# Optimization experiments

Hardware: AMD Instinct MI355X
Metric: run time of the kernel (lower is better)

Reference implementation:

```python
import jax, jax.numpy as jnp
import numpy as np


def setup_inputs() -> dict:
    key = jax.random.key(0)
    x = jax.random.normal(key, (4096, 16384), dtype=jnp.float32)
    return {"x": x, "k": 64}


def reference(x, k):
    # TopK activation: keep the k largest-|value| entries per row, zero the rest.
    if k <= 0:
        return jnp.zeros_like(x)
    kk = min(k, x.shape[-1])
    _, idx = jax.lax.top_k(jnp.abs(x), kk)          # idx: [rows, kk]
    rows = jnp.arange(x.shape[0])[:, None]          # [rows, 1]
    mask = jnp.zeros_like(x).at[rows, idx].set(1.0)  # scatter ones at top-k positions
    return x * mask
```

## Files before the change

kernel.cpp:

```cpp
#include <hip/hip_runtime.h>

#define ROW_LEN 16384
#define THREADS 256
#define ITERS (ROW_LEN / (THREADS * 4))
#define NBINS 2048
#define CAP 1024
#define MBCAP 128
#define TPRE 2.5f

typedef float f4v __attribute__((ext_vector_type(4)));

__device__ __forceinline__ unsigned long long make_key(unsigned abits, unsigned idx) {
    return ((unsigned long long)abits << 32) | (unsigned)(~idx);
}

__device__ __forceinline__ void find_boundary(const unsigned* hist, unsigned kk,
                                              int* s_b, unsigned* s_g, unsigned* wtot) {
    const int t = threadIdx.x;
    const int lane = t & 63;
    const int w = t >> 6;
    unsigned s_own = 0;
    #pragma unroll
    for (int i = 0; i < 8; ++i) s_own += hist[t * 8 + i];
    unsigned acc = s_own;
    #pragma unroll
    for (int off = 1; off < 64; off <<= 1) {
        unsigned v = __shfl_down(acc, off);
        if (lane + off < 64) acc += v;
    }
    if (lane == 0) wtot[w] = acc;
    __syncthreads();
    unsigned addw = 0;
    #pragma unroll
    for (int w2 = 0; w2 < THREADS / 64; ++w2) if (w2 > w) addw += wtot[w2];
    unsigned above = acc - s_own + addw;
    #pragma unroll
    for (int i = 7; i >= 0; --i) {
        unsigned h = hist[t * 8 + i];
        if (above < kk && above + h >= kk) { *s_b = t * 8 + i; *s_g = above; }
        above += h;
    }
    __syncthreads();
}

__global__ __launch_bounds__(THREADS)
void topk_act_kernel(const float* __restrict__ x, const int* __restrict__ kptr,
                     float* __restrict__ out)
{
    const int t = threadIdx.x;
    const long long row = blockIdx.x;
    const f4v* __restrict__ xv = (const f4v*)(x + row * ROW_LEN);
    f4v* __restrict__ ov = (f4v*)(out + row * ROW_LEN);

    const int k = *kptr;
    if (k <= 0) {
        f4v z = (f4v)(0.0f);
        #pragma unroll
        for (int j = 0; j < ITERS; ++j)
            __builtin_nontemporal_store(z, &ov[j * THREADS + t]);
        return;
    }
    const unsigned kk = (unsigned)(k < ROW_LEN ? k : ROW_LEN);

    __shared__ unsigned hist[NBINS];
    __shared__ unsigned long long lst[CAP];
    __shared__ unsigned long long lst2[MBCAP];
    __shared__ unsigned wtot[THREADS / 64];
    __shared__ unsigned s_cnt, s_cnt2;
    __shared__ int s_b;
    __shared__ unsigned s_g;
    __shared__ unsigned long long s_ccut;

    if (t == 0) { s_cnt = 0u; s_cnt2 = 0u; }
    __syncthreads();

    const unsigned abs_pre = __float_as_uint(TPRE);
    for (int it = 0; it < ITERS; ++it) {
        f4v v = xv[it * THREADS + t];
        #pragma unroll
        for (int c = 0; c < 4; ++c) {
            unsigned ab = __float_as_uint(v[c]) & 0x7fffffffu;
            if (ab >= abs_pre) {
                unsigned p = atomicAdd(&s_cnt, 1u);
                if (p < CAP) {
                    unsigned idx = (unsigned)((it * THREADS + t) * 4 + c);
                    lst[p] = make_key(ab, idx);
                }
            }
        }
    }
    __syncthreads();

    const unsigned m_all = s_cnt;

    if (m_all >= kk && m_all <= CAP) {
        for (int i = t; i < NBINS; i += THREADS) hist[i] = 0u;
        __syncthreads();
        for (unsigned e = t; e < m_all; e += THREADS) {
            float a = __uint_as_float((unsigned)(lst[e] >> 32));
            int rb = (int)((a - TPRE) * 1024.0f);
            rb = rb > (NBINS - 1) ? (NBINS - 1) : rb;
            atomicAdd(&hist[rb], 1u);
        }
        __syncthreads();
        find_boundary(hist, kk, &s_b, &s_g, wtot);
        const int bsel = s_b;
        const unsigned r = kk - s_g;
        for (unsigned e = t; e < m_all; e += THREADS) {
            unsigned long long key = lst[e];
            float a = __uint_as_float((unsigned)(key >> 32));
            int rb = (int)((a - TPRE) * 1024.0f);
            rb = rb > (NBINS - 1) ? (NBINS - 1) : rb;
            if (rb == bsel) {
                unsigned p = atomicAdd(&s_cnt2, 1u);
                if (p < MBCAP) lst2[p] = key;
            }
        }
        __syncthreads();
        const unsigned mb = s_cnt2;
        if (mb <= MBCAP) {
            for (unsigned e = t; e < mb; e += THREADS) {
                unsigned long long ce = lst2[e];
                unsigned rank = 0;
                for (unsigned q = 0; q < mb; ++q) rank += (lst2[q] > ce) ? 1u : 0u;
                if (rank == r - 1) s_ccut = ce;
            }
        } else {
            for (unsigned e = t; e < m_all; e += THREADS) {
                unsigned long long ce = lst[e];
                float a = __uint_as_float((unsigned)(ce >> 32));
                int rb = (int)((a - TPRE) * 1024.0f);
                rb = rb > (NBINS - 1) ? (NBINS - 1) : rb;
                if (rb == bsel) {
                    unsigned rank = 0;
                    for (unsigned q = 0; q < m_all; ++q) {
                        unsigned long long kq = lst[q];
                        float aq = __uint_as_float((unsigned)(kq >> 32));
                        int rbq = (int)((aq - TPRE) * 1024.0f);
                        rbq = rbq > (NBINS - 1) ? (NBINS - 1) : rbq;
                        rank += (rbq == bsel && kq > ce) ? 1u : 0u;
                    }
                    if (rank == r - 1) s_ccut = ce;
                }
            }
        }
        __syncthreads();
    } else {
        for (int i = t; i < NBINS; i += THREADS) hist[i] = 0u;
        if (t == 0) s_cnt = 0u;
        __syncthreads();
        for (int it = 0; it < ITERS; ++it) {
            f4v v = xv[it * THREADS + t];
            #pragma unroll
            for (int c = 0; c < 4; ++c) {
                float a = fabsf(v[c]);
                int bin = (int)(a * 256.0f);
                bin = bin > (NBINS - 1) ? (NBINS - 1) : bin;
                atomicAdd(&hist[bin], 1u);
            }
        }
        __syncthreads();
        find_boundary(hist, kk, &s_b, &s_g, wtot);
        const int b = s_b;
        unsigned r = kk - s_g;
        for (int it = 0; it < ITERS; ++it) {
            f4v v = xv[it * THREADS + t];
            #pragma unroll
            for (int c = 0; c < 4; ++c) {
                unsigned ab = __float_as_uint(v[c]) & 0x7fffffffu;
                float a = __uint_as_float(ab);
                int bin = (int)(a * 256.0f);
                bin = bin > (NBINS - 1) ? (NBINS - 1) : bin;
                if (bin == b) {
                    unsigned p = atomicAdd(&s_cnt, 1u);
                    if (p < CAP) {
                        unsigned idx = (unsigned)((it * THREADS + t) * 4 + c);
                        lst[p] = make_key(ab, idx);
                    }
                }
            }
        }
        __syncthreads();
        const unsigned mbf = s_cnt < CAP ? s_cnt : CAP;
        if (r > mbf) r = mbf;
        for (unsigned e = t; e < mbf; e += THREADS) {
            unsigned long long ce = lst[e];
            unsigned rank = 0;
            for (unsigned q = 0; q < mbf; ++q) rank += (lst[q] > ce) ? 1u : 0u;
            if (rank == r - 1) s_ccut = ce;
        }
        __syncthreads();
    }

    const unsigned long long cc = s_ccut;
    const unsigned cut_hi = (unsigned)(cc >> 32);
    const unsigned cut_lo = (unsigned)cc;

    for (int it = 0; it < ITERS; ++it) {
        f4v v = xv[it * THREADS + t];
        f4v w;
        #pragma unroll
        for (int c = 0; c < 4; ++c) {
            unsigned ab = __float_as_uint(v[c]) & 0x7fffffffu;
            unsigned idx = (unsigned)((it * THREADS + t) * 4 + c);
            bool keep = (ab > cut_hi) | ((ab == cut_hi) & (~idx >= cut_lo));
            w[c] = keep ? v[c] : 0.0f;
        }
        __builtin_nontemporal_store(w, &ov[it * THREADS + t]);
    }
}

extern "C" void kernel_launch(void* const* d_in, const int* in_sizes, int n_in,
                              void* d_out, int out_size, void* d_ws, size_t ws_size,
                              hipStream_t stream) {
    const float* x  = (const float*)d_in[0];
    const int*   kp = (const int*)d_in[1];
    float* out = (float*)d_out;
    const int rows = out_size / ROW_LEN;
    topk_act_kernel<<<dim3(rows), dim3(THREADS), 0, stream>>>(x, kp, out);
}
```

Before: 464.5 us.

## Cache each row in registers once and reuse across all passes

Measured after the change: 503.6 us. 1.08x slower.

```diff
diff --git a/kernel.cpp b/kernel.cpp
--- a/kernel.cpp
+++ b/kernel.cpp
@@ -43,7 +43,7 @@
     __syncthreads();
 }
 
-__global__ __launch_bounds__(THREADS)
+__global__ __launch_bounds__(THREADS, 4)
 void topk_act_kernel(const float* __restrict__ x, const int* __restrict__ kptr,
                      float* __restrict__ out)
 {
@@ -71,15 +71,22 @@
     __shared__ unsigned s_g;
     __shared__ unsigned long long s_ccut;
 
+    f4v vals[ITERS];
+    #pragma unroll
+    for (int it = 0; it < ITERS; ++it)
+        vals[it] = __builtin_nontemporal_load(&xv[it * THREADS + t]);
+
+    #pragma unroll
+    for (int i = 0; i < NBINS / THREADS; ++i) hist[i * THREADS + t] = 0u;
     if (t == 0) { s_cnt = 0u; s_cnt2 = 0u; }
     __syncthreads();
 
     const unsigned abs_pre = __float_as_uint(TPRE);
+    #pragma unroll
     for (int it = 0; it < ITERS; ++it) {
-        f4v v = xv[it * THREADS + t];
         #pragma unroll
         for (int c = 0; c < 4; ++c) {
-            unsigned ab = __float_as_uint(v[c]) & 0x7fffffffu;
+            unsigned ab = __float_as_uint(vals[it][c]) & 0x7fffffffu;
             if (ab >= abs_pre) {
                 unsigned p = atomicAdd(&s_cnt, 1u);
                 if (p < CAP) {
@@ -94,8 +101,6 @@
     const unsigned m_all = s_cnt;
 
     if (m_all >= kk && m_all <= CAP) {
-        for (int i = t; i < NBINS; i += THREADS) hist[i] = 0u;
-        __syncthreads();
         for (unsigned e = t; e < m_all; e += THREADS) {
             float a = __uint_as_float((unsigned)(lst[e] >> 32));
             int rb = (int)((a - TPRE) * 1024.0f);
@@ -146,14 +151,11 @@
         }
         __syncthreads();
     } else {
-        for (int i = t; i < NBINS; i += THREADS) hist[i] = 0u;
-        if (t == 0) s_cnt = 0u;
-        __syncthreads();
+        #pragma unroll
         for (int it = 0; it < ITERS; ++it) {
-            f4v v = xv[it * THREADS + t];
             #pragma unroll
             for (int c = 0; c < 4; ++c) {
-                float a = fabsf(v[c]);
+                float a = fabsf(vals[it][c]);
                 int bin = (int)(a * 256.0f);
                 bin = bin > (NBINS - 1) ? (NBINS - 1) : bin;
                 atomicAdd(&hist[bin], 1u);
@@ -163,16 +165,16 @@
         find_boundary(hist, kk, &s_b, &s_g, wtot);
         const int b = s_b;
         unsigned r = kk - s_g;
+        #pragma unroll
         for (int it = 0; it < ITERS; ++it) {
-            f4v v = xv[it * THREADS + t];
             #pragma unroll
             for (int c = 0; c < 4; ++c) {
-                unsigned ab = __float_as_uint(v[c]) & 0x7fffffffu;
+                unsigned ab = __float_as_uint(vals[it][c]) & 0x7fffffffu;
                 float a = __uint_as_float(ab);
                 int bin = (int)(a * 256.0f);
                 bin = bin > (NBINS - 1) ? (NBINS - 1) : bin;
                 if (bin == b) {
-                    unsigned p = atomicAdd(&s_cnt, 1u);
+                    unsigned p = atomicAdd(&s_cnt2, 1u);
                     if (p < CAP) {
                         unsigned idx = (unsigned)((it * THREADS + t) * 4 + c);
                         lst[p] = make_key(ab, idx);
@@ -181,7 +183,7 @@
             }
         }
         __syncthreads();
-        const unsigned mbf = s_cnt < CAP ? s_cnt : CAP;
+        const unsigned mbf = s_cnt2 < CAP ? s_cnt2 : CAP;
         if (r > mbf) r = mbf;
         for (unsigned e = t; e < mbf; e += THREADS) {
             unsigned long long ce = lst[e];
@@ -196,15 +198,15 @@
     const unsigned cut_hi = (unsigned)(cc >> 32);
     const unsigned cut_lo = (unsigned)cc;
 
+    #pragma unroll
     for (int it = 0; it < ITERS; ++it) {
-        f4v v = xv[it * THREADS + t];
         f4v w;
         #pragma unroll
         for (int c = 0; c < 4; ++c) {
-            unsigned ab = __float_as_uint(v[c]) & 0x7fffffffu;
+            unsigned ab = __float_as_uint(vals[it][c]) & 0x7fffffffu;
             unsigned idx = (unsigned)((it * THREADS + t) * 4 + c);
             bool keep = (ab > cut_hi) | ((ab == cut_hi) & (~idx >= cut_lo));
-            w[c] = keep ? v[c] : 0.0f;
+            w[c] = keep ? vals[it][c] : 0.0f;
         }
         __builtin_nontemporal_store(w, &ov[it * THREADS + t]);
     }
```
